# Kernel tuning notes

Measured on AMD Instinct MI355X. Metric: run time of the kernel, lower is better.

Reference implementation:

```python
import jax, jax.numpy as jnp
import numpy as np

N_NODES = 25000
N_EDGES = 400000
N_GRAPHS = 100
D_IN = 16
D = 32          # node_dim
K = 11          # spectral coefficients = edge_dim
NOUT1 = 30
NOUT2 = 2
L = 2           # n_interactions
D_OUT = 32


def setup_inputs() -> dict:
    key = jax.random.key(0)
    ks = jax.random.split(key, 24)
    s = 0.1
    inp = {
        'x': jax.random.normal(ks[0], (N_NODES, D_IN), jnp.float32),
        'edge_attr': jax.random.uniform(ks[1], (N_EDGES, K), jnp.float32),
        'edge_index': jax.random.randint(ks[2], (2, N_EDGES), 0, N_NODES),
        'batch': jnp.sort(jax.random.randint(ks[3], (N_NODES,), 0, N_GRAPHS)),
        # embedding
        'emb_w': jax.random.normal(ks[4], (D_IN, D)) * s,
        'emb_b': jnp.zeros((D,)),
        # per-interaction params, stacked on leading L axis
        'init_w': jax.random.normal(ks[5], (L, D, D)) * s,             # initial_dense (no bias)
        'e1_w': jax.random.normal(ks[6], (L, K, 2 * K)) * s,
        'e2_w': jax.random.normal(ks[7], (L, K, 2 * K)) * s,
        'e3_w': jax.random.normal(ks[8], (L, K, 2 * K)) * s,
        'e4_w': jax.random.normal(ks[9], (L, 4 * K, K)) * s,
        'conv_w': jax.random.normal(ks[10], (L, K, D, NOUT1)) * s,     # SpectConv weight (selfconn=False)
        'conv_b': jnp.zeros((L, NOUT1)),
        'att_v': jax.random.normal(ks[11], (L, D, 1)) * s,
        'skip1_w': jax.random.normal(ks[12], (L, D, NOUT2)) * s,
        'skip1_b': jnp.full((L, NOUT2), 0.01),
        'skip2_w': jax.random.normal(ks[13], (L, D, NOUT2)) * s,
        'skip2_b': jnp.full((L, NOUT2), 0.01),
        'out_w': jax.random.normal(ks[14], (L, NOUT1 + NOUT2, D)) * s,
        'out_b': jnp.full((L, D), 0.01),
        # encoder output head
        'final_w': jax.random.normal(ks[15], (D, D_OUT)) * s,
        'final_b': jnp.zeros((D_OUT,)),
    }
    return inp


def _segment_softmax(raw, dst, n):
    m = jax.ops.segment_max(raw, dst, num_segments=n)
    m = jnp.where(jnp.isfinite(m), m, 0.0)
    e = jnp.exp(raw - m[dst])
    denom = jax.ops.segment_sum(e, dst, num_segments=n)
    return e / (denom[dst] + 1e-16)


def _interaction(h, src, dst, edge_attr, p):
    (init_w, e1_w, e2_w, e3_w, e4_w, conv_w, conv_b, att_v,
     s1_w, s1_b, s2_w, s2_b, out_w, out_b) = p
    n = h.shape[0]
    h_proj = h @ init_w                                     # [N, D]
    # learned edge transform
    lin = jax.nn.relu(edge_attr @ e1_w)                     # [E, 2K]
    gate = jnp.tanh(edge_attr @ e2_w) * jnp.tanh(edge_attr @ e3_w)
    ea = jax.nn.relu(jnp.concatenate([lin, gate], axis=1) @ e4_w)  # [E, K]
    # spectral conv with attention (selfconn=False)
    xs = h_proj[src]                                        # gather [E, D]
    msgs = ea[:, :, None] * xs[:, None, :]                  # [E, K, D]
    agg = jax.ops.segment_sum(msgs, dst, num_segments=n)    # [N, K, D]
    sum_out = jnp.einsum('nkd,kdo->no', agg, conv_w)        # [N, NOUT1]
    pooled = ea.mean(axis=1, keepdims=True) * xs            # mean_k msg_k, [E, D]
    raw_att = (pooled @ att_v)[:, 0]                        # [E]
    att = _segment_softmax(raw_att, dst, n)                 # [E]
    att_agg = jax.ops.segment_sum(att[:, None, None] * msgs, dst, num_segments=n)
    att_out = jnp.einsum('nkd,kdo->no', att_agg, conv_w)
    conv_out = jax.nn.relu(sum_out + att_out + conv_b)      # [N, NOUT1]
    skip = jnp.tanh(h_proj @ s1_w + s1_b) * jnp.tanh(h_proj @ s2_w + s2_b)  # [N, NOUT2]
    layer_out = jnp.concatenate([conv_out, skip], axis=1)
    delta = layer_out @ out_w + out_b                       # [N, D]
    return delta, att


def reference(x, edge_attr, emb_w, emb_b, init_w, e1_w, e2_w, e3_w, e4_w,
              conv_w, conv_b, att_v, skip1_w, skip1_b, skip2_w, skip2_b,
              out_w, out_b, final_w, final_b, edge_index, batch):
    src, dst = edge_index[0], edge_index[1]
    h = x @ emb_w + emb_b                                   # node embedding [N, D]
    atts = []
    for l in range(L):
        p = (init_w[l], e1_w[l], e2_w[l], e3_w[l], e4_w[l], conv_w[l], conv_b[l],
             att_v[l], skip1_w[l], skip1_b[l], skip2_w[l], skip2_b[l], out_w[l], out_b[l])
        delta, att = _interaction(h, src, dst, edge_attr, p)
        h = h + delta                                       # residual
        atts.append(att)
    # global mean pool per graph
    counts = jax.ops.segment_sum(jnp.ones((h.shape[0],), h.dtype), batch, num_segments=N_GRAPHS)
    pooled = jax.ops.segment_sum(h, batch, num_segments=N_GRAPHS) / jnp.maximum(counts, 1.0)[:, None]
    output = pooled @ final_w + final_b                     # [G, D_OUT]
    return output, h, jnp.stack(atts)
```

## Files before the change

### kernel.cpp

```cpp
#include <hip/hip_runtime.h>
#include <hip/hip_bf16.h>

typedef __hip_bfloat16 bf16;
using f32x4v = __attribute__((ext_vector_type(4))) float;
using bf16x8 = __attribute__((ext_vector_type(8))) short;

#define N_NODES 25000
#define N_PAD   25024
#define N_EDGES 400000
#define N_GR    100

__device__ __forceinline__ bf16 tob(float v) { return __float2bfloat16(v); }
__device__ __forceinline__ unsigned short tobu(float v) {
  union { bf16 b; unsigned short u; } c; c.b = __float2bfloat16(v); return c.u;
}
__device__ __forceinline__ float b2f(unsigned short u) { return __uint_as_float(((unsigned)u) << 16); }
__device__ __forceinline__ float tanh_fast(float x) {
  float e = __expf(2.f * x);
  return 1.f - 2.f * __builtin_amdgcn_rcpf(e + 1.f);
}

__global__ __launch_bounds__(256) void hist_kernel(const int* __restrict__ dst, int* __restrict__ deg, int E) {
  int e = blockIdx.x * blockDim.x + threadIdx.x;
  if (e < E) atomicAdd(&deg[dst[e]], 1);
}

__global__ __launch_bounds__(1024) void scan_kernel(const int* __restrict__ deg, int* __restrict__ offs,
                                                    int* __restrict__ cur, int n) {
  __shared__ int wsum[16];
  __shared__ int wpre[16];
  int t = threadIdx.x, lane = t & 63, w = t >> 6;
  int carry = 0;
  for (int base = 0; base < n; base += 1024) {
    int v = (base + t < n) ? deg[base + t] : 0;
    int x = v;
    #pragma unroll
    for (int s = 1; s < 64; s <<= 1) { int y = __shfl_up(x, s); if (lane >= s) x += y; }
    if (lane == 63) wsum[w] = x;
    __syncthreads();
    if (w == 0 && lane < 16) {
      int ws_ = wsum[lane];
      int xs = ws_;
      #pragma unroll
      for (int s = 1; s < 16; s <<= 1) { int y = __shfl_up(xs, s); if (lane >= s) xs += y; }
      wpre[lane] = xs - ws_;
    }
    __syncthreads();
    int excl = carry + wpre[w] + x - v;
    if (base + t < n) { offs[base + t] = excl; cur[base + t] = excl; }
    carry += wpre[15] + wsum[15];
    __syncthreads();
  }
  if (t == 0) offs[n] = carry;
}

__global__ __launch_bounds__(256) void fill_kernel(const int* __restrict__ dst, int* __restrict__ cur,
                                                   int* __restrict__ elist, int* __restrict__ epos, int E) {
  int e = blockIdx.x * blockDim.x + threadIdx.x;
  if (e < E) { int p = atomicAdd(&cur[dst[e]], 1); elist[p] = e; epos[e] = p; }
}

__global__ __launch_bounds__(256) void prep_kernel(const float* __restrict__ e1, const float* __restrict__ e2,
                                                   const float* __restrict__ e3, const float* __restrict__ e4,
                                                   const float* __restrict__ attv, const float* __restrict__ convw,
                                                   const float* __restrict__ outw,
                                                   const int* __restrict__ batch,
                                                   float* __restrict__ wE, bf16* __restrict__ Wt,
                                                   bf16* __restrict__ owB, int* __restrict__ gb) {
  int i = blockIdx.x * blockDim.x + threadIdx.x;
  if (i < 2 * 1352) {
    int l = i / 1352, r = i % 1352;
    float v = 0.f;
    if (r < 264)       { int q = r;        int j = q / 12, k = q % 12; if (k < 11) v = e1[l*242 + k*22 + j]; }
    else if (r < 528)  { int q = r - 264;  int j = q / 12, k = q % 12; if (k < 11) v = e2[l*242 + k*22 + j]; }
    else if (r < 792)  { int q = r - 528;  int j = q / 12, k = q % 12; if (k < 11) v = e3[l*242 + k*22 + j]; }
    else if (r < 1056) { int q = r - 792;  int j = q / 12, k = q % 12; if (k < 11) v = e4[l*484 + j*11 + k]; }
    else if (r < 1320) { int q = r - 1056; int j = q / 12, k = q % 12; if (k < 11) v = e4[l*484 + (22 + j)*11 + k]; }
    else               { int d = r - 1320; v = attv[l*32 + d]; }
    wE[i] = v;
  }
  int t = i - 2 * 1352;
  if (t >= 0 && t < 2 * 32 * 352) {
    int l = t / (32 * 352), q = t % (32 * 352);
    int o = q / 352, dk = q % 352;
    int d = dk / 11, kk = dk % 11;
    float v = 0.f;
    if (o < 30) v = convw[l*10560 + (kk*32 + d)*30 + o];
    Wt[t] = tob(v);
  }
  int u = i - 2 * 1352 - 2 * 32 * 352;
  if (u >= 0 && u < 2048) {
    int l = u >> 10, rem = u & 1023;
    int hf = rem >> 9, rem2 = rem & 511;
    int lane = rem2 >> 3, j = rem2 & 7;
    int k = (lane >> 4) * 8 + j, n = lane & 15;
    owB[u] = tob(outw[l*1024 + k*32 + hf*16 + n]);
  }
  int g = i - 2 * 1352 - 2 * 32 * 352 - 2048;
  if (g >= 0 && g <= N_GR) {
    if (g == N_GR) { gb[g] = N_NODES; }
    else {
      int lo = 0, hi = N_NODES;
      while (lo < hi) { int mid = (lo + hi) >> 1; if (batch[mid] < g) lo = mid + 1; else hi = mid; }
      gb[g] = lo;
    }
  }
}

__global__ __launch_bounds__(256) void emb_hproj_kernel(const float* __restrict__ x, const float* __restrict__ w,
                                                        const float* __restrict__ b, const float* __restrict__ w1,
                                                        float* __restrict__ h, float* __restrict__ hp,
                                                        unsigned short* __restrict__ hpb, int N) {
  __shared__ float semb[16 * 32];
  __shared__ float sw1[32 * 32];
  __shared__ float sb[32];
  __shared__ float sx[8][16];
  __shared__ float sh[8][33];
  int tid = threadIdx.x;
  for (int i = tid; i < 16 * 32; i += 256) semb[i] = w[i];
  for (int i = tid; i < 32 * 32; i += 256) sw1[i] = w1[i];
  if (tid < 32) sb[tid] = b[tid];
  int nb = blockIdx.x * 8;
  if (tid < 128) {
    int n = nb + (tid >> 4), k = tid & 15;
    sx[tid >> 4][k] = (n < N) ? x[(size_t)n * 16 + k] : 0.f;
  }
  __syncthreads();
  int grp = tid >> 5, d = tid & 31;
  int n = nb + grp;
  float acc = sb[d];
  #pragma unroll
  for (int k = 0; k < 16; k++) acc += sx[grp][k] * semb[k*32 + d];
  sh[grp][d] = acc;
  if (n < N) h[(size_t)n * 32 + d] = acc;
  __syncthreads();
  float hpv = 0.f;
  #pragma unroll
  for (int k = 0; k < 32; k++) hpv += sh[grp][k] * sw1[k*32 + d];
  if (n < N) {
    hp[(size_t)n * 32 + d] = hpv;
    hpb[(size_t)n * 32 + d] = tobu(hpv);
  }
}

__device__ __forceinline__ void loadw12(const float4* base, int idx3, float* w) {
  float4 a = base[idx3], b = base[idx3 + 1], c = base[idx3 + 2];
  w[0]=a.x; w[1]=a.y; w[2]=a.z; w[3]=a.w;
  w[4]=b.x; w[5]=b.y; w[6]=b.z; w[7]=b.w;
  w[8]=c.x; w[9]=c.y; w[10]=c.z; w[11]=c.w;
}

__global__ __launch_bounds__(256) void edge_kernel(const float* __restrict__ eattr,
                                                   const int* __restrict__ srcA,
                                                   const int* __restrict__ epos,
                                                   const unsigned short* __restrict__ hpb,
                                                   const float* __restrict__ wEl,
                                                   uint4* __restrict__ pay, int E) {
  const float4* w4 = (const float4*)wEl;
  int e = blockIdx.x * blockDim.x + threadIdx.x;
  bool live = e < E;
  float a[11], acc[11];
  #pragma unroll
  for (int k = 0; k < 11; k++) {
    a[k] = live ? eattr[(size_t)e*11 + k] : 0.f;
    acc[k] = 0.f;
  }
  for (int j = 0; j < 22; j++) {
    float w[12];
    loadw12(w4, j*3, w);
    float l1 = 0.f;
    #pragma unroll
    for (int k = 0; k < 11; k++) l1 += a[k] * w[k];
    loadw12(w4, 66 + j*3, w);
    float l2 = 0.f;
    #pragma unroll
    for (int k = 0; k < 11; k++) l2 += a[k] * w[k];
    loadw12(w4, 132 + j*3, w);
    float l3 = 0.f;
    #pragma unroll
    for (int k = 0; k < 11; k++) l3 += a[k] * w[k];
    float gg = tanh_fast(l2) * tanh_fast(l3);
    l1 = fmaxf(l1, 0.f);
    float wl[12], wg[12];
    loadw12(w4, 198 + j*3, wl);
    loadw12(w4, 264 + j*3, wg);
    #pragma unroll
    for (int k = 0; k < 11; k++) acc[k] += l1*wl[k] + gg*wg[k];
  }
  if (!live) return;
  const float* av = wEl + 1320;
  float mean = 0.f;
  #pragma unroll
  for (int k = 0; k < 11; k++) { acc[k] = fmaxf(acc[k], 0.f); mean += acc[k]; }
  mean *= (1.f / 11.f);
  int s = srcA[e];
  const uint2* hb = (const uint2*)(hpb + (size_t)s * 32);
  float dot = 0.f;
  #pragma unroll
  for (int q = 0; q < 8; q++) {
    uint2 hv = hb[q];
    dot += b2f((unsigned short)hv.x) * av[q*4+0] + b2f((unsigned short)(hv.x >> 16)) * av[q*4+1]
         + b2f((unsigned short)hv.y) * av[q*4+2] + b2f((unsigned short)(hv.y >> 16)) * av[q*4+3];
  }
  float raw = mean * dot;
  unsigned p[6];
  #pragma unroll
  for (int q = 0; q < 5; q++)
    p[q] = (unsigned)tobu(acc[2*q]) | ((unsigned)tobu(acc[2*q+1]) << 16);
  p[5] = (unsigned)tobu(acc[10]);
  int pp = epos[e];
  pay[(size_t)pp * 2]     = make_uint4(p[0], p[1], p[2], p[3]);
  pay[(size_t)pp * 2 + 1] = make_uint4(p[4], p[5], __float_as_uint(raw), (unsigned)s);
}

__device__ __forceinline__ void unpack_pay(uint4 p0, uint4 p1, float* ev) {
  ev[0] = b2f((unsigned short)p0.x); ev[1] = b2f((unsigned short)(p0.x >> 16));
  ev[2] = b2f((unsigned short)p0.y); ev[3] = b2f((unsigned short)(p0.y >> 16));
  ev[4] = b2f((unsigned short)p0.z); ev[5] = b2f((unsigned short)(p0.z >> 16));
  ev[6] = b2f((unsigned short)p0.w); ev[7] = b2f((unsigned short)(p0.w >> 16));
  ev[8] = b2f((unsigned short)p1.x); ev[9] = b2f((unsigned short)(p1.x >> 16));
  ev[10] = b2f((unsigned short)p1.y);
}

__global__ __launch_bounds__(256) void node_kernel(const int* __restrict__ offs, const int* __restrict__ elist,
                                                   const uint4* __restrict__ pay,
                                                   const unsigned short* __restrict__ hpb,
                                                   bf16* __restrict__ Abuf, float* __restrict__ atts, int N) {
  int wid = threadIdx.x >> 6, lane = threadIdx.x & 63;
  int half = lane >> 5, d = lane & 31;
  int n = blockIdx.x * 4 + wid;
  if (n >= N_PAD) return;
  int beg = 0, deg = 0;
  if (n < N) { beg = offs[n]; deg = offs[n + 1] - beg; }
  const float* payf = (const float*)pay;

  float m_l = -1e30f;
  for (int jj = lane; jj < deg; jj += 64)
    m_l = fmaxf(m_l, payf[(size_t)(beg + jj) * 8 + 6]);
  #pragma unroll
  for (int s = 1; s < 64; s <<= 1) m_l = fmaxf(m_l, __shfl_xor(m_l, s));
  float M = m_l;

  float s_l = 0.f;
  for (int jj = lane; jj < deg; jj += 64)
    s_l += __expf(payf[(size_t)(beg + jj) * 8 + 6] - M);
  #pragma unroll
  for (int s = 1; s < 64; s <<= 1) s_l += __shfl_xor(s_l, s);
  float inv = 1.f / (s_l + 1e-16f);

  for (int jj = lane; jj < deg; jj += 64) {
    float r = payf[(size_t)(beg + jj) * 8 + 6];
    atts[elist[beg + jj]] = __expf(r - M) * inv;
  }

  float agg[11];
  #pragma unroll
  for (int k = 0; k < 11; k++) agg[k] = 0.f;

  int j = half;
  for (; j + 2 < deg; j += 4) {
    uint4 a0 = pay[(size_t)(beg + j) * 2],     a1 = pay[(size_t)(beg + j) * 2 + 1];
    uint4 b0 = pay[(size_t)(beg + j + 2) * 2], b1 = pay[(size_t)(beg + j + 2) * 2 + 1];
    float xa = b2f(hpb[(size_t)(int)a1.w * 32 + d]);
    float xb = b2f(hpb[(size_t)(int)b1.w * 32 + d]);
    float ca = 1.f + __expf(__uint_as_float(a1.z) - M) * inv;
    float cb = 1.f + __expf(__uint_as_float(b1.z) - M) * inv;
    float cxa = ca * xa, cxb = cb * xb;
    float eva[11], evb[11];
    unpack_pay(a0, a1, eva);
    unpack_pay(b0, b1, evb);
    #pragma unroll
    for (int k = 0; k < 11; k++) agg[k] += eva[k] * cxa + evb[k] * cxb;
  }
  for (; j < deg; j += 2) {
    uint4 q0 = pay[(size_t)(beg + j) * 2], q1 = pay[(size_t)(beg + j) * 2 + 1];
    float xs = b2f(hpb[(size_t)(int)q1.w * 32 + d]);
    float c = 1.f + __expf(__uint_as_float(q1.z) - M) * inv;
    float cx = c * xs;
    float ev[11];
    unpack_pay(q0, q1, ev);
    #pragma unroll
    for (int k = 0; k < 11; k++) agg[k] += ev[k] * cx;
  }

  #pragma unroll
  for (int k = 0; k < 11; k++) agg[k] += __shfl_xor(agg[k], 32);

  if (half == 0) {
    bf16* arow = Abuf + (size_t)n * 352 + d * 11;
    #pragma unroll
    for (int k = 0; k < 11; k++) arow[k] = tob(agg[k]);
  }
}

__global__ __launch_bounds__(256) void convfused_kernel(const short* __restrict__ A, const short* __restrict__ Wt,
                                                        const short* __restrict__ owB,
                                                        const float* __restrict__ hp, float* __restrict__ h,
                                                        const float* __restrict__ convb,
                                                        const float* __restrict__ s1w, const float* __restrict__ s1b,
                                                        const float* __restrict__ s2w, const float* __restrict__ s2b,
                                                        const float* __restrict__ outb,
                                                        const float* __restrict__ initw_next,
                                                        float* __restrict__ hp_out, unsigned short* __restrict__ hpb_out,
                                                        int N) {
  __shared__ short slo[64][40];
  __shared__ float sdelta[64][36];
  __shared__ float sskipw[128];
  __shared__ float sskipb[4];
  __shared__ float scb[32];
  __shared__ float sob[32];
  __shared__ float sw1[1024];
  int tid = threadIdx.x;
  if (tid < 64) sskipw[tid] = s1w[tid];
  if (tid >= 64 && tid < 128) sskipw[tid] = s2w[tid - 64];
  if (tid >= 128 && tid < 160) sob[tid - 128] = outb[tid - 128];
  if (tid >= 160 && tid < 192) scb[tid - 160] = (tid - 160 < 30) ? convb[tid - 160] : 0.f;
  if (tid >= 192 && tid < 196) sskipb[tid - 192] = (tid < 194) ? s1b[tid - 192] : s2b[tid - 194];
  if (initw_next) {
    for (int i = tid; i < 1024; i += 256) sw1[i] = initw_next[i];
  }
  __syncthreads();

  int wave = tid >> 6, lane = tid & 63;
  int r16 = lane & 15, kq = lane >> 4;
  int mbase = blockIdx.x * 64 + wave * 16;

  const short* arow = A + (size_t)(mbase + r16) * 352 + kq * 8;
  const short* b0p = Wt + (size_t)r16 * 352 + kq * 8;
  const short* b1p = b0p + 16 * 352;
  f32x4v acc0 = {0.f, 0.f, 0.f, 0.f}, acc1 = {0.f, 0.f, 0.f, 0.f};
  #pragma unroll
  for (int ks = 0; ks < 11; ks++) {
    bf16x8 af = *(const bf16x8*)(arow + ks * 32);
    bf16x8 b0 = *(const bf16x8*)(b0p + ks * 32);
    bf16x8 b1 = *(const bf16x8*)(b1p + ks * 32);
    acc0 = __builtin_amdgcn_mfma_f32_16x16x32_bf16(af, b0, acc0, 0, 0, 0);
    acc1 = __builtin_amdgcn_mfma_f32_16x16x32_bf16(af, b1, acc1, 0, 0, 0);
  }
  #pragma unroll
  for (int r = 0; r < 4; r++) {
    int row = wave * 16 + kq * 4 + r;
    slo[row][r16] = (short)tobu(fmaxf(acc0[r] + scb[r16], 0.f));
    if (r16 < 14) slo[row][16 + r16] = (short)tobu(fmaxf(acc1[r] + scb[16 + r16], 0.f));
  }
  __syncthreads();

  if (tid < 128) {
    int row = tid >> 1, jx = tid & 1;
    int grow = blockIdx.x * 64 + row;
    float a1 = sskipb[jx], a2 = sskipb[2 + jx];
    if (grow < N) {
      const float* hr = hp + (size_t)grow * 32;
      #pragma unroll
      for (int dd = 0; dd < 32; dd++) {
        float hv = hr[dd];
        a1 += hv * sskipw[dd*2 + jx];
        a2 += hv * sskipw[64 + dd*2 + jx];
      }
    }
    slo[row][30 + jx] = (short)tobu(tanh_fast(a1) * tanh_fast(a2));
  }
  __syncthreads();

  bf16x8 a2f = *(const bf16x8*)&slo[wave * 16 + r16][kq * 8];
  bf16x8 bo0 = *(const bf16x8*)(owB + lane * 8);
  bf16x8 bo1 = *(const bf16x8*)(owB + 512 + lane * 8);
  f32x4v d0 = {0.f, 0.f, 0.f, 0.f}, d1 = {0.f, 0.f, 0.f, 0.f};
  d0 = __builtin_amdgcn_mfma_f32_16x16x32_bf16(a2f, bo0, d0, 0, 0, 0);
  d1 = __builtin_amdgcn_mfma_f32_16x16x32_bf16(a2f, bo1, d1, 0, 0, 0);
  #pragma unroll
  for (int r = 0; r < 4; r++) {
    int row = wave * 16 + kq * 4 + r;
    sdelta[row][r16] = d0[r] + sob[r16];
    sdelta[row][16 + r16] = d1[r] + sob[16 + r16];
  }
  __syncthreads();

  int row = tid >> 2, col0 = (tid & 3) * 8;
  int grow = blockIdx.x * 64 + row;
  if (grow < N) {
    float* hr = h + (size_t)grow * 32 + col0;
    float4 ha = *(float4*)hr;
    float4 hb = *(float4*)(hr + 4);
    float4 da = *(float4*)&sdelta[row][col0];
    float4 db = *(float4*)&sdelta[row][col0 + 4];
    ha.x += da.x; ha.y += da.y; ha.z += da.z; ha.w += da.w;
    hb.x += db.x; hb.y += db.y; hb.z += db.z; hb.w += db.w;
    *(float4*)hr = ha;
    *(float4*)(hr + 4) = hb;
    *(float4*)&sdelta[row][col0] = ha;
    *(float4*)&sdelta[row][col0 + 4] = hb;
  }
  if (initw_next) {
    __syncthreads();
    if (grow < N) {
      float o[8];
      #pragma unroll
      for (int c = 0; c < 8; c++) o[c] = 0.f;
      #pragma unroll
      for (int k = 0; k < 32; k++) {
        float hv = sdelta[row][k];
        #pragma unroll
        for (int c = 0; c < 8; c++) o[c] += hv * sw1[k*32 + col0 + c];
      }
      float* hpo = hp_out + (size_t)grow * 32 + col0;
      unsigned short* hbo = hpb_out + (size_t)grow * 32 + col0;
      #pragma unroll
      for (int c = 0; c < 8; c++) { hpo[c] = o[c]; hbo[c] = tobu(o[c]); }
    }
  }
}

__global__ __launch_bounds__(256) void pool2_kernel(const float* __restrict__ h, const int* __restrict__ gb,
                                                    const float* __restrict__ fw, const float* __restrict__ fb,
                                                    float* __restrict__ out0, float* __restrict__ outh) {
  __shared__ float part[8][32];
  __shared__ float pooled[32];
  int g = blockIdx.x;
  int s = gb[g], e = gb[g + 1];
  int grp = threadIdx.x >> 5, d = threadIdx.x & 31;
  float acc = 0.f;
  for (int n = s + grp; n < e; n += 8) {
    float v = h[(size_t)n * 32 + d];
    outh[(size_t)n * 32 + d] = v;
    acc += v;
  }
  part[grp][d] = acc;
  __syncthreads();
  if (threadIdx.x < 32) {
    float sum = 0.f;
    #pragma unroll
    for (int i = 0; i < 8; i++) sum += part[i][d];
    pooled[d] = sum / fmaxf((float)(e - s), 1.f);
  }
  __syncthreads();
  if (threadIdx.x < 32) {
    int jx = threadIdx.x;
    float o = fb[jx];
    #pragma unroll
    for (int dd = 0; dd < 32; dd++) o += pooled[dd] * fw[dd*32 + jx];
    out0[g * 32 + jx] = o;
  }
}

extern "C" void kernel_launch(void* const* d_in, const int* in_sizes, int n_in,
                              void* d_out, int out_size, void* d_ws, size_t ws_size,
                              hipStream_t stream) {
  (void)in_sizes; (void)n_in; (void)out_size; (void)ws_size;
  const float* x      = (const float*)d_in[0];
  const float* eattr  = (const float*)d_in[1];
  const int* eidx     = (const int*)d_in[2];
  const int* batch    = (const int*)d_in[3];
  const float* emb_w  = (const float*)d_in[4];
  const float* emb_b  = (const float*)d_in[5];
  const float* init_w = (const float*)d_in[6];
  const float* e1w    = (const float*)d_in[7];
  const float* e2w    = (const float*)d_in[8];
  const float* e3w    = (const float*)d_in[9];
  const float* e4w    = (const float*)d_in[10];
  const float* convw  = (const float*)d_in[11];
  const float* convb  = (const float*)d_in[12];
  const float* attv   = (const float*)d_in[13];
  const float* s1w    = (const float*)d_in[14];
  const float* s1b    = (const float*)d_in[15];
  const float* s2w    = (const float*)d_in[16];
  const float* s2b    = (const float*)d_in[17];
  const float* outw   = (const float*)d_in[18];
  const float* outb   = (const float*)d_in[19];
  const float* finw   = (const float*)d_in[20];
  const float* finb   = (const float*)d_in[21];

  char* ws = (char*)d_ws;
  size_t off = 0;
  auto take = [&](size_t bytes) -> char* {
    char* p = ws + off;
    off += (bytes + 255) & ~(size_t)255;
    return p;
  };
  float* h    = (float*)take((size_t)N_NODES * 32 * 4);
  float* hp   = (float*)take((size_t)N_NODES * 32 * 4);
  unsigned short* hpb = (unsigned short*)take((size_t)N_NODES * 32 * 2);
  uint4* pay  = (uint4*)take((size_t)N_EDGES * 32);
  bf16*  Abuf = (bf16*)take((size_t)N_PAD * 352 * 2);
  int*   deg  = (int*)take((size_t)N_NODES * 4);
  int*   offs = (int*)take((size_t)(N_NODES + 1) * 4);
  int*   cur  = (int*)take((size_t)N_NODES * 4);
  int*   elist= (int*)take((size_t)N_EDGES * 4);
  int*   epos = (int*)take((size_t)N_EDGES * 4);
  int*   gb   = (int*)take((size_t)(N_GR + 1) * 4);
  float* wE   = (float*)take((size_t)2 * 1352 * 4);
  bf16*  Wt   = (bf16*)take((size_t)2 * 32 * 352 * 2);
  bf16*  owB  = (bf16*)take((size_t)2048 * 2);

  float* out0 = (float*)d_out;
  float* outh = out0 + N_GR * 32;
  float* outa = outh + (size_t)N_NODES * 32;

  const int* srcA = eidx;
  const int* dstA = eidx + N_EDGES;

  hipMemsetAsync(deg, 0, (size_t)N_NODES * 4, stream);

  prep_kernel<<<107, 256, 0, stream>>>(e1w, e2w, e3w, e4w, attv, convw, outw, batch, wE, Wt, owB, gb);
  hist_kernel<<<(N_EDGES + 255) / 256, 256, 0, stream>>>(dstA, deg, N_EDGES);
  scan_kernel<<<1, 1024, 0, stream>>>(deg, offs, cur, N_NODES);
  fill_kernel<<<(N_EDGES + 255) / 256, 256, 0, stream>>>(dstA, cur, elist, epos, N_EDGES);
  emb_hproj_kernel<<<(N_NODES + 7) / 8, 256, 0, stream>>>(x, emb_w, emb_b, init_w, h, hp, hpb, N_NODES);

  for (int l = 0; l < 2; l++) {
    edge_kernel<<<(N_EDGES + 255) / 256, 256, 0, stream>>>(
        eattr, srcA, epos, hpb, wE + l * 1352, pay, N_EDGES);
    node_kernel<<<N_PAD / 4, 256, 0, stream>>>(offs, elist, pay, hpb,
                                               Abuf, outa + (size_t)l * N_EDGES, N_NODES);
    convfused_kernel<<<N_PAD / 64, 256, 0, stream>>>(
        (const short*)Abuf, (const short*)Wt + (size_t)l * 32 * 352, (const short*)owB + (size_t)l * 1024,
        hp, h, convb + l * 30, s1w + l * 64, s1b + l * 2, s2w + l * 64, s2b + l * 2,
        outb + l * 32,
        (l == 0) ? (init_w + 1024) : nullptr, hp, hpb, N_NODES);
  }

  pool2_kernel<<<N_GR, 256, 0, stream>>>(h, gb, finw, finb, out0, outh);
}
```

Before: 246.5 us.

## Fuse CSR fill into edge kernel, single-pass scan, fast softmax, smaller conv blocks

Several independent changes. The CSR fill step moves into the first-layer edge kernel, and zeroing deg moves into prep_kernel in place of the memset, which removes two launches. The scan kernel becomes a single pass where each thread sums a chunk of 25 elements serially. The node kernel gains a fast path for degree at most 64 that keeps the softmax weights in registers and reads them with shuffles instead of recomputing exp. The conv kernel uses 32-row blocks of 128 threads to get more blocks. The atomic fill order is nondeterministic as before, but it now shares the edge kernel and may lengthen that kernel's critical path.

```diff
diff --git a/kernel.cpp b/kernel.cpp
--- a/kernel.cpp
+++ b/kernel.cpp
@@ -9,6 +9,7 @@
 #define N_PAD   25024
 #define N_EDGES 400000
 #define N_GR    100
+#define SCAN_C  25
 
 __device__ __forceinline__ bf16 tob(float v) { return __float2bfloat16(v); }
 __device__ __forceinline__ unsigned short tobu(float v) {
@@ -30,34 +31,34 @@
   __shared__ int wsum[16];
   __shared__ int wpre[16];
   int t = threadIdx.x, lane = t & 63, w = t >> 6;
-  int carry = 0;
-  for (int base = 0; base < n; base += 1024) {
-    int v = (base + t < n) ? deg[base + t] : 0;
-    int x = v;
-    #pragma unroll
-    for (int s = 1; s < 64; s <<= 1) { int y = __shfl_up(x, s); if (lane >= s) x += y; }
-    if (lane == 63) wsum[w] = x;
-    __syncthreads();
-    if (w == 0 && lane < 16) {
-      int ws_ = wsum[lane];
-      int xs = ws_;
-      #pragma unroll
-      for (int s = 1; s < 16; s <<= 1) { int y = __shfl_up(xs, s); if (lane >= s) xs += y; }
-      wpre[lane] = xs - ws_;
-    }
-    __syncthreads();
-    int excl = carry + wpre[w] + x - v;
-    if (base + t < n) { offs[base + t] = excl; cur[base + t] = excl; }
-    carry += wpre[15] + wsum[15];
-    __syncthreads();
-  }
-  if (t == 0) offs[n] = carry;
-}
-
-__global__ __launch_bounds__(256) void fill_kernel(const int* __restrict__ dst, int* __restrict__ cur,
-                                                   int* __restrict__ elist, int* __restrict__ epos, int E) {
-  int e = blockIdx.x * blockDim.x + threadIdx.x;
-  if (e < E) { int p = atomicAdd(&cur[dst[e]], 1); elist[p] = e; epos[e] = p; }
+  int base = t * SCAN_C;
+  int loc[SCAN_C];
+  int s = 0;
+  #pragma unroll
+  for (int i = 0; i < SCAN_C; i++) {
+    int idx = base + i;
+    int v = (idx < n) ? deg[idx] : 0;
+    loc[i] = s; s += v;
+  }
+  int x = s;
+  #pragma unroll
+  for (int sh = 1; sh < 64; sh <<= 1) { int y = __shfl_up(x, sh); if (lane >= sh) x += y; }
+  if (lane == 63) wsum[w] = x;
+  __syncthreads();
+  if (w == 0 && lane < 16) {
+    int ws_ = wsum[lane], xs = ws_;
+    #pragma unroll
+    for (int sh = 1; sh < 16; sh <<= 1) { int y = __shfl_up(xs, sh); if (lane >= sh) xs += y; }
+    wpre[lane] = xs - ws_;
+  }
+  __syncthreads();
+  int excl = wpre[w] + x - s;
+  #pragma unroll
+  for (int i = 0; i < SCAN_C; i++) {
+    int idx = base + i;
+    if (idx < n) { int o = excl + loc[i]; offs[idx] = o; cur[idx] = o; }
+  }
+  if (t == 1023) offs[n] = excl + s;
 }
 
 __global__ __launch_bounds__(256) void prep_kernel(const float* __restrict__ e1, const float* __restrict__ e2,
@@ -66,8 +67,10 @@
                                                    const float* __restrict__ outw,
                                                    const int* __restrict__ batch,
                                                    float* __restrict__ wE, bf16* __restrict__ Wt,
-                                                   bf16* __restrict__ owB, int* __restrict__ gb) {
+                                                   bf16* __restrict__ owB, int* __restrict__ gb,
+                                                   int* __restrict__ deg) {
   int i = blockIdx.x * blockDim.x + threadIdx.x;
+  if (i < N_NODES) deg[i] = 0;
   if (i < 2 * 1352) {
     int l = i / 1352, r = i % 1352;
     float v = 0.f;
@@ -152,10 +155,13 @@
 
 __global__ __launch_bounds__(256) void edge_kernel(const float* __restrict__ eattr,
                                                    const int* __restrict__ srcA,
-                                                   const int* __restrict__ epos,
+                                                   const int* __restrict__ dstA,
+                                                   int* __restrict__ cur,
+                                                   int* __restrict__ elist,
+                                                   int* __restrict__ epos,
                                                    const unsigned short* __restrict__ hpb,
                                                    const float* __restrict__ wEl,
-                                                   uint4* __restrict__ pay, int E) {
+                                                   uint4* __restrict__ pay, int first, int E) {
   const float4* w4 = (const float4*)wEl;
   int e = blockIdx.x * blockDim.x + threadIdx.x;
   bool live = e < E;
@@ -164,6 +170,16 @@
   for (int k = 0; k < 11; k++) {
     a[k] = live ? eattr[(size_t)e*11 + k] : 0.f;
     acc[k] = 0.f;
+  }
+  int pp = 0;
+  if (live) {
+    if (first) {
+      pp = atomicAdd(&cur[dstA[e]], 1);
+      elist[pp] = e;
+      epos[e] = pp;
+    } else {
+      pp = epos[e];
+    }
   }
   for (int j = 0; j < 22; j++) {
     float w[12];
@@ -208,7 +224,6 @@
   for (int q = 0; q < 5; q++)
     p[q] = (unsigned)tobu(acc[2*q]) | ((unsigned)tobu(acc[2*q+1]) << 16);
   p[5] = (unsigned)tobu(acc[10]);
-  int pp = epos[e];
   pay[(size_t)pp * 2]     = make_uint4(p[0], p[1], p[2], p[3]);
   pay[(size_t)pp * 2 + 1] = make_uint4(p[4], p[5], __float_as_uint(raw), (unsigned)s);
 }
@@ -234,23 +249,39 @@
   if (n < N) { beg = offs[n]; deg = offs[n + 1] - beg; }
   const float* payf = (const float*)pay;
 
-  float m_l = -1e30f;
-  for (int jj = lane; jj < deg; jj += 64)
-    m_l = fmaxf(m_l, payf[(size_t)(beg + jj) * 8 + 6]);
-  #pragma unroll
-  for (int s = 1; s < 64; s <<= 1) m_l = fmaxf(m_l, __shfl_xor(m_l, s));
-  float M = m_l;
-
-  float s_l = 0.f;
-  for (int jj = lane; jj < deg; jj += 64)
-    s_l += __expf(payf[(size_t)(beg + jj) * 8 + 6] - M);
-  #pragma unroll
-  for (int s = 1; s < 64; s <<= 1) s_l += __shfl_xor(s_l, s);
-  float inv = 1.f / (s_l + 1e-16f);
-
-  for (int jj = lane; jj < deg; jj += 64) {
-    float r = payf[(size_t)(beg + jj) * 8 + 6];
-    atts[elist[beg + jj]] = __expf(r - M) * inv;
+  float M, inv;
+  float einv_reg = 0.f;
+  bool fast = (deg <= 64);
+  if (fast) {
+    float r = (lane < deg) ? payf[(size_t)(beg + lane) * 8 + 6] : -1e30f;
+    float mm = r;
+    #pragma unroll
+    for (int sh = 1; sh < 64; sh <<= 1) mm = fmaxf(mm, __shfl_xor(mm, sh));
+    M = mm;
+    float ex = (lane < deg) ? __expf(r - M) : 0.f;
+    float ss = ex;
+    #pragma unroll
+    for (int sh = 1; sh < 64; sh <<= 1) ss += __shfl_xor(ss, sh);
+    inv = 1.f / (ss + 1e-16f);
+    einv_reg = ex * inv;
+    if (lane < deg) atts[elist[beg + lane]] = einv_reg;
+  } else {
+    float m_l = -1e30f;
+    for (int jj = lane; jj < deg; jj += 64)
+      m_l = fmaxf(m_l, payf[(size_t)(beg + jj) * 8 + 6]);
+    #pragma unroll
+    for (int sh = 1; sh < 64; sh <<= 1) m_l = fmaxf(m_l, __shfl_xor(m_l, sh));
+    M = m_l;
+    float s_l = 0.f;
+    for (int jj = lane; jj < deg; jj += 64)
+      s_l += __expf(payf[(size_t)(beg + jj) * 8 + 6] - M);
+    #pragma unroll
+    for (int sh = 1; sh < 64; sh <<= 1) s_l += __shfl_xor(s_l, sh);
+    inv = 1.f / (s_l + 1e-16f);
+    for (int jj = lane; jj < deg; jj += 64) {
+      float r = payf[(size_t)(beg + jj) * 8 + 6];
+      atts[elist[beg + jj]] = __expf(r - M) * inv;
+    }
   }
 
   float agg[11];
@@ -263,8 +294,10 @@
     uint4 b0 = pay[(size_t)(beg + j + 2) * 2], b1 = pay[(size_t)(beg + j + 2) * 2 + 1];
     float xa = b2f(hpb[(size_t)(int)a1.w * 32 + d]);
     float xb = b2f(hpb[(size_t)(int)b1.w * 32 + d]);
-    float ca = 1.f + __expf(__uint_as_float(a1.z) - M) * inv;
-    float cb = 1.f + __expf(__uint_as_float(b1.z) - M) * inv;
+    float ca = fast ? (1.f + __shfl(einv_reg, j))
+                    : (1.f + __expf(__uint_as_float(a1.z) - M) * inv);
+    float cb = fast ? (1.f + __shfl(einv_reg, j + 2))
+                    : (1.f + __expf(__uint_as_float(b1.z) - M) * inv);
     float cxa = ca * xa, cxb = cb * xb;
     float eva[11], evb[11];
     unpack_pay(a0, a1, eva);
@@ -275,7 +308,8 @@
   for (; j < deg; j += 2) {
     uint4 q0 = pay[(size_t)(beg + j) * 2], q1 = pay[(size_t)(beg + j) * 2 + 1];
     float xs = b2f(hpb[(size_t)(int)q1.w * 32 + d]);
-    float c = 1.f + __expf(__uint_as_float(q1.z) - M) * inv;
+    float c = fast ? (1.f + __shfl(einv_reg, j))
+                   : (1.f + __expf(__uint_as_float(q1.z) - M) * inv);
     float cx = c * xs;
     float ev[11];
     unpack_pay(q0, q1, ev);
@@ -293,7 +327,7 @@
   }
 }
 
-__global__ __launch_bounds__(256) void convfused_kernel(const short* __restrict__ A, const short* __restrict__ Wt,
+__global__ __launch_bounds__(128) void convfused_kernel(const short* __restrict__ A, const short* __restrict__ Wt,
                                                         const short* __restrict__ owB,
                                                         const float* __restrict__ hp, float* __restrict__ h,
                                                         const float* __restrict__ convb,
@@ -303,8 +337,8 @@
                                                         const float* __restrict__ initw_next,
                                                         float* __restrict__ hp_out, unsigned short* __restrict__ hpb_out,
                                                         int N) {
-  __shared__ short slo[64][40];
-  __shared__ float sdelta[64][36];
+  __shared__ short slo[32][40];
+  __shared__ float sdelta[32][36];
   __shared__ float sskipw[128];
   __shared__ float sskipb[4];
   __shared__ float scb[32];
@@ -313,17 +347,17 @@
   int tid = threadIdx.x;
   if (tid < 64) sskipw[tid] = s1w[tid];
   if (tid >= 64 && tid < 128) sskipw[tid] = s2w[tid - 64];
-  if (tid >= 128 && tid < 160) sob[tid - 128] = outb[tid - 128];
-  if (tid >= 160 && tid < 192) scb[tid - 160] = (tid - 160 < 30) ? convb[tid - 160] : 0.f;
-  if (tid >= 192 && tid < 196) sskipb[tid - 192] = (tid < 194) ? s1b[tid - 192] : s2b[tid - 194];
+  if (tid < 32) sob[tid] = outb[tid];
+  if (tid >= 32 && tid < 64) scb[tid - 32] = (tid - 32 < 30) ? convb[tid - 32] : 0.f;
+  if (tid >= 96 && tid < 100) sskipb[tid - 96] = (tid < 98) ? s1b[tid - 96] : s2b[tid - 98];
   if (initw_next) {
-    for (int i = tid; i < 1024; i += 256) sw1[i] = initw_next[i];
+    for (int i = tid; i < 1024; i += 128) sw1[i] = initw_next[i];
   }
   __syncthreads();
 
   int wave = tid >> 6, lane = tid & 63;
   int r16 = lane & 15, kq = lane >> 4;
-  int mbase = blockIdx.x * 64 + wave * 16;
+  int mbase = blockIdx.x * 32 + wave * 16;
 
   const short* arow = A + (size_t)(mbase + r16) * 352 + kq * 8;
   const short* b0p = Wt + (size_t)r16 * 352 + kq * 8;
@@ -345,9 +379,9 @@
   }
   __syncthreads();
 
-  if (tid < 128) {
+  if (tid < 64) {
     int row = tid >> 1, jx = tid & 1;
-    int grow = blockIdx.x * 64 + row;
+    int grow = blockIdx.x * 32 + row;
     float a1 = sskipb[jx], a2 = sskipb[2 + jx];
     if (grow < N) {
       const float* hr = hp + (size_t)grow * 32;
@@ -377,7 +411,7 @@
   __syncthreads();
 
   int row = tid >> 2, col0 = (tid & 3) * 8;
-  int grow = blockIdx.x * 64 + row;
+  int grow = blockIdx.x * 32 + row;
   if (grow < N) {
     float* hr = h + (size_t)grow * 32 + col0;
     float4 ha = *(float4*)hr;
@@ -499,20 +533,17 @@
   const int* srcA = eidx;
   const int* dstA = eidx + N_EDGES;
 
-  hipMemsetAsync(deg, 0, (size_t)N_NODES * 4, stream);
-
-  prep_kernel<<<107, 256, 0, stream>>>(e1w, e2w, e3w, e4w, attv, convw, outw, batch, wE, Wt, owB, gb);
+  prep_kernel<<<107, 256, 0, stream>>>(e1w, e2w, e3w, e4w, attv, convw, outw, batch, wE, Wt, owB, gb, deg);
   hist_kernel<<<(N_EDGES + 255) / 256, 256, 0, stream>>>(dstA, deg, N_EDGES);
   scan_kernel<<<1, 1024, 0, stream>>>(deg, offs, cur, N_NODES);
-  fill_kernel<<<(N_EDGES + 255) / 256, 256, 0, stream>>>(dstA, cur, elist, epos, N_EDGES);
   emb_hproj_kernel<<<(N_NODES + 7) / 8, 256, 0, stream>>>(x, emb_w, emb_b, init_w, h, hp, hpb, N_NODES);
 
   for (int l = 0; l < 2; l++) {
     edge_kernel<<<(N_EDGES + 255) / 256, 256, 0, stream>>>(
-        eattr, srcA, epos, hpb, wE + l * 1352, pay, N_EDGES);
+        eattr, srcA, dstA, cur, elist, epos, hpb, wE + l * 1352, pay, (l == 0) ? 1 : 0, N_EDGES);
     node_kernel<<<N_PAD / 4, 256, 0, stream>>>(offs, elist, pay, hpb,
                                                Abuf, outa + (size_t)l * N_EDGES, N_NODES);
-    convfused_kernel<<<N_PAD / 64, 256, 0, stream>>>(
+    convfused_kernel<<<N_PAD / 32, 128, 0, stream>>>(
         (const short*)Abuf, (const short*)Wt + (size_t)l * 32 * 352, (const short*)owB + (size_t)l * 1024,
         hp, h, convb + l * 30, s1w + l * 64, s1b + l * 2, s2w + l * 64, s2b + l * 2,
         outb + l * 32,
```

Measured after the change: 231.0 us. 1.07x faster.
